# Kernel optimization log

Measured on AMD Instinct MI355X. Metric: run time of the kernel, lower is better.

The kernel has to match this reference:

```python
import jax, jax.numpy as jnp
import numpy as np

B, T, D, H, C = 2048, 512, 5, 128, 10  # batch, seq_len, input_dim, hidden_dim, num_classes


def setup_inputs() -> dict:
    key = jax.random.key(0)
    ks = jax.random.split(key, 13)
    s = 1.0 / np.sqrt(H)  # PyTorch LSTM init range

    def u(k, shape):
        return jax.random.uniform(k, shape, jnp.float32, -s, s)

    return {
        "x": jax.random.normal(ks[0], (B, T, D), jnp.float32),
        # layer 0 (gate order i,f,g,o as in PyTorch)
        "w_ih0": u(ks[1], (4 * H, D)),
        "w_hh0": u(ks[2], (4 * H, H)),
        "b_ih0": u(ks[3], (4 * H,)),
        "b_hh0": u(ks[4], (4 * H,)),
        # layer 1
        "w_ih1": u(ks[5], (4 * H, H)),
        "w_hh1": u(ks[6], (4 * H, H)),
        "b_ih1": u(ks[7], (4 * H,)),
        "b_hh1": u(ks[8], (4 * H,)),
        # classifier: Linear(H, H//2) -> ReLU -> Linear(H//2, C); dropout inactive (eval)
        "cw1": u(ks[9], (H // 2, H)),
        "cb1": u(ks[10], (H // 2,)),
        "cw2": u(ks[11], (C, H // 2)),
        "cb2": u(ks[12], (C,)),
    }


def _lstm_layer(xs, w_ih, w_hh, b_ih, b_hh):
    # xs: [T, B, in]; returns (ys [T, B, H], h_T [B, H])
    Hh = w_hh.shape[1]
    b = b_ih + b_hh

    def step(carry, x_t):
        h, c = carry
        gates = x_t @ w_ih.T + h @ w_hh.T + b  # [B, 4H]
        i, f, g, o = jnp.split(gates, 4, axis=-1)
        c = jax.nn.sigmoid(f) * c + jax.nn.sigmoid(i) * jnp.tanh(g)
        h = jax.nn.sigmoid(o) * jnp.tanh(c)
        return (h, c), h

    Bn = xs.shape[1]
    h0 = jnp.zeros((Bn, Hh), xs.dtype)
    (h_T, _), ys = jax.lax.scan(step, (h0, h0), xs)
    return ys, h_T


def reference(x, w_ih0, w_hh0, b_ih0, b_hh0, w_ih1, w_hh1, b_ih1, b_hh1, cw1, cb1, cw2, cb2):
    xs = jnp.transpose(x, (1, 0, 2))  # [T, B, D]
    ys0, _ = _lstm_layer(xs, w_ih0, w_hh0, b_ih0, b_hh0)
    # inter-layer dropout(0.2) is a no-op in eval mode
    _, last_hidden = _lstm_layer(ys0, w_ih1, w_hh1, b_ih1, b_hh1)  # h_n[-1]: [B, H]
    # classifier (Dropout(0.3) inactive in eval)
    r = jax.nn.relu(last_hidden @ cw1.T + cb1)
    output = r @ cw2.T + cb2  # [B, C]
    return (output, last_hidden)
```

## Files before the change

kernel.cpp:

```cpp
#include <hip/hip_runtime.h>

typedef unsigned short ushort;
typedef unsigned int uint;
typedef __bf16 bf16_t;
typedef bf16_t bf16x8 __attribute__((ext_vector_type(8)));
typedef float f32x4 __attribute__((ext_vector_type(4)));

#define B_ 2048
#define T_ 512
#define D_ 5
#define H_ 128
#define C_ 10
#define BT 16
#define BLK 512
#define NP 128
#define CH 8
#define H0STR 168
#define H1STR 136
#define SSTR 136
#define XSTR 40

static __device__ __forceinline__ float b2f(ushort u) {
    return __builtin_bit_cast(float, ((uint)u) << 16);
}
static __device__ __forceinline__ ushort f2b(float f) {
    uint u = __builtin_bit_cast(uint, f);
    u += 0x7FFFu + ((u >> 16) & 1u);
    return (ushort)(u >> 16);
}
static __device__ __forceinline__ float sigf(float x) {
    return __builtin_amdgcn_rcpf(1.0f + __expf(-x));
}
static __device__ __forceinline__ float tanhf_(float x) {
    return 1.0f - 2.0f * __builtin_amdgcn_rcpf(1.0f + __expf(2.0f * x));
}
static __device__ __forceinline__ float ldf(const void* p, long i, bool m32) {
    return m32 ? ((const float*)p)[i] : b2f(((const ushort*)p)[i]);
}
static __device__ __forceinline__ bf16x8 ld16(const ushort* p) {
    return __builtin_bit_cast(bf16x8, *(const uint4*)p);
}
static __device__ __forceinline__ bf16x8 ldfrag(const void* p, long idx, bool m32) {
    if (!m32) return ld16((const ushort*)p + idx);
    const float* f = (const float*)p + idx;
    union { ushort u[8]; bf16x8 v; } r;
#pragma unroll
    for (int j = 0; j < 8; ++j) r.u[j] = f2b(f[j]);
    return r.v;
}
static __device__ __forceinline__ f32x4 splat4(float v) {
    f32x4 r = {v, v, v, v};
    return r;
}
static __device__ __forceinline__ int swz(int row, int col) {
    return row * SSTR + ((((col >> 4) ^ (row >> 3)) << 4) | (col & 15));
}
static __device__ __forceinline__ void bar_lds() {
    asm volatile("s_waitcnt lgkmcnt(0)" ::: "memory");
    __builtin_amdgcn_s_barrier();
    asm volatile("" ::: "memory");
}

__global__ void detect_dtype(const ushort* __restrict__ w, int* __restrict__ flag) {
    __shared__ int cnt;
    if (threadIdx.x == 0) cnt = 0;
    __syncthreads();
    int local = 0;
    for (int i = threadIdx.x; i < 16384; i += 256)
        if ((uint)(w[i] & 0x7F80u) >= 0x4180u) ++local;
    atomicAdd(&cnt, local);
    __syncthreads();
    if (threadIdx.x == 0) *flag = (cnt > 512) ? 1 : 0;
}

__global__ void init_flags(int* __restrict__ prog) {
    prog[threadIdx.x] = 0;
}

__global__ __launch_bounds__(BLK, 2) void lstm2_pipe(
    const void* __restrict__ x,
    const void* __restrict__ wih0, const void* __restrict__ whh0,
    const void* __restrict__ bih0, const void* __restrict__ bhh0,
    const void* __restrict__ wih1, const void* __restrict__ whh1,
    const void* __restrict__ bih1, const void* __restrict__ bhh1,
    const void* __restrict__ cw1, const void* __restrict__ cb1,
    const void* __restrict__ cw2, const void* __restrict__ cb2,
    const int* __restrict__ flag,
    ushort* __restrict__ fifo, int* __restrict__ prog_p, int* __restrict__ prog_c,
    int F, void* __restrict__ out)
{
    __shared__ __align__(16) ushort sA[2][BT * SSTR];
    __shared__ __align__(16) ushort sB[2][BT * SSTR];
    __shared__ __align__(16) ushort xch[CH * 16 * XSTR];
    __shared__ float rs[BT * 64];

    const bool m32 = (*flag) != 0;
    const int tid  = threadIdx.x;
    const int w    = tid >> 6;
    const int lane = tid & 63;
    const int quad = lane >> 4;
    const int l16  = lane & 15;

    if ((int)blockIdx.x < NP) {
        const int p   = blockIdx.x;
        const int bt0 = p * BT;
        ushort* myfifo = fifo + (long)p * F * (BT * H_);

        const int e0 = tid;
        const int r0 = e0 / 40, rem0 = e0 - r0 * 40;
        const int tt0 = rem0 / 5, d0 = rem0 - tt0 * 5;
        const long xo0 = (long)(bt0 + r0) * T_ * D_ + (long)tt0 * D_ + d0;
        const int xdst0 = (tt0 * 16 + r0) * XSTR + d0;
        const int e1 = tid + 512;
        const int r1 = e1 / 40, rem1 = e1 - r1 * 40;
        const int tt1 = rem1 / 5, d1 = rem1 - tt1 * 5;
        const long xo1 = (long)(bt0 + r1) * T_ * D_ + (long)tt1 * D_ + d1;
        const int xdst1 = (tt1 * 16 + r1) * XSTR + d1;
        const bool has1 = (tid < 128);

        for (int i = tid; i < CH * 16 * XSTR; i += BLK) xch[i] = 0;

        bf16x8 wh0c[4][4];
        bf16x8 xbf[4];
        float  b0v[4];
#pragma unroll
        for (int g = 0; g < 4; ++g) {
            const int n = g * 128 + w * 16 + l16;
#pragma unroll
            for (int kt = 0; kt < 4; ++kt)
                wh0c[g][kt] = ldfrag(whh0, (long)n * 128 + kt * 32 + quad * 8, m32);
            union { ushort u[8]; bf16x8 v; } xt;
#pragma unroll
            for (int j = 0; j < 8; ++j) xt.u[j] = 0;
            if (quad == 0) {
#pragma unroll
                for (int j = 0; j < 5; ++j) xt.u[j] = f2b(ldf(wih0, (long)n * D_ + j, m32));
            }
            xbf[g] = xt.v;
            b0v[g] = ldf(bih0, n, m32) + ldf(bhh0, n, m32);
        }
        __syncthreads();

        {
            float v0 = ldf(x, xo0, m32);
            float v1 = has1 ? ldf(x, xo1, m32) : 0.f;
            xch[xdst0] = f2b(v0);
            if (has1) xch[xdst1] = f2b(v1);
        }
        float xp0 = ldf(x, xo0 + (long)(CH * D_), m32);
        float xp1 = has1 ? ldf(x, xo1 + (long)(CH * D_), m32) : 0.f;
        __syncthreads();

        bf16x8 h0f[4];
        {
            uint4 z = make_uint4(0, 0, 0, 0);
            h0f[0] = h0f[1] = h0f[2] = h0f[3] = __builtin_bit_cast(bf16x8, z);
        }
        f32x4 c0 = splat4(0.f);

#pragma unroll 1
        for (int t = 0; t < T_; ++t) {
            const int wb = (t + 1) & 1;
            if ((t & (CH - 1)) == 0 && t > 0) {
                __syncthreads();
                xch[xdst0] = f2b(xp0);
                if (has1) xch[xdst1] = f2b(xp1);
                if (tid == 0) {
                    __hip_atomic_store(&prog_p[p], t, __ATOMIC_RELEASE,
                                       __HIP_MEMORY_SCOPE_AGENT);
                    int need = t + CH - F;
                    if (need > 0)
                        while (__hip_atomic_load(&prog_c[p], __ATOMIC_RELAXED,
                                                 __HIP_MEMORY_SCOPE_AGENT) < need)
                            __builtin_amdgcn_s_sleep(2);
                }
                __syncthreads();
                const int tb = t + CH;
                xp0 = (tb + tt0 < T_) ? ldf(x, xo0 + (long)tb * D_, m32) : 0.f;
                xp1 = (has1 && tb + tt1 < T_) ? ldf(x, xo1 + (long)tb * D_, m32) : 0.f;
            }

            f32x4 a[4];
#pragma unroll
            for (int g = 0; g < 4; ++g) a[g] = splat4(b0v[g]);
#pragma unroll
            for (int kt = 0; kt < 4; ++kt)
#pragma unroll
                for (int g = 0; g < 4; ++g)
                    a[g] = __builtin_amdgcn_mfma_f32_16x16x32_bf16(
                        h0f[kt], wh0c[g][kt], a[g], 0, 0, 0);
            {
                bf16x8 ha4 = ld16(&xch[((t & (CH - 1)) * 16 + l16) * XSTR + quad * 8]);
#pragma unroll
                for (int g = 0; g < 4; ++g)
                    a[g] = __builtin_amdgcn_mfma_f32_16x16x32_bf16(
                        ha4, xbf[g], a[g], 0, 0, 0);
            }
            ushort* fs = myfifo + (long)(t & (F - 1)) * (BT * H_);
#pragma unroll
            for (int r = 0; r < 4; ++r) {
                float iv = sigf(a[0][r]), fv = sigf(a[1][r]);
                float gv = tanhf_(a[2][r]), ov = sigf(a[3][r]);
                float cv = fv * c0[r] + iv * gv;
                c0[r] = cv;
                ushort hv = f2b(ov * tanhf_(cv));
                int row = quad * 4 + r;
                sA[wb][swz(row, w * 16 + l16)] = hv;
                fs[row * H_ + w * 16 + l16] = hv;
            }
            bar_lds();
#pragma unroll
            for (int kt = 0; kt < 4; ++kt)
                h0f[kt] = ld16(&sA[wb][swz(l16, kt * 32 + quad * 8)]);
        }
        __syncthreads();
        if (tid == 0)
            __hip_atomic_store(&prog_p[p], T_, __ATOMIC_RELEASE,
                               __HIP_MEMORY_SCOPE_AGENT);
    } else {
        const int p   = blockIdx.x - NP;
        const int bt0 = p * BT;
        const ushort* myfifo = fifo + (long)p * F * (BT * H_);

        for (int i = tid; i < BT * SSTR; i += BLK) sB[0][i] = 0;

        bf16x8 wi1f[4][4], wh1f[4][4];
        float  b1v[4];
#pragma unroll
        for (int g = 0; g < 4; ++g) {
            const int n = g * 128 + w * 16 + l16;
#pragma unroll
            for (int kt = 0; kt < 4; ++kt) {
                wi1f[g][kt] = ldfrag(wih1, (long)n * 128 + kt * 32 + quad * 8, m32);
                wh1f[g][kt] = ldfrag(whh1, (long)n * 128 + kt * 32 + quad * 8, m32);
            }
            b1v[g] = ldf(bih1, n, m32) + ldf(bhh1, n, m32);
        }

        if (tid == 0) {
            while (__hip_atomic_load(&prog_p[p], __ATOMIC_RELAXED,
                                     __HIP_MEMORY_SCOPE_AGENT) < 2 * CH)
                __builtin_amdgcn_s_sleep(2);
            __builtin_amdgcn_fence(__ATOMIC_ACQUIRE, "agent");
        }
        __syncthreads();
        {
            int row = tid >> 5, col4 = (tid & 31) * 4;
            uint2 d = *(const uint2*)(myfifo + tid * 4);
            *(uint2*)&sA[0][swz(row, col4)] = d;
        }
        __syncthreads();

        f32x4 c1 = splat4(0.f);

#pragma unroll 1
        for (int t = 0; t < T_; ++t) {
            const int rb = t & 1, wb = (t + 1) & 1;
            if (((t + 1) & (CH - 1)) == 0 && t + 1 < T_) {
                if (tid == 0) {
                    int target = t + 1 + CH;
                    if (target > T_) target = T_;
                    while (__hip_atomic_load(&prog_p[p], __ATOMIC_RELAXED,
                                             __HIP_MEMORY_SCOPE_AGENT) < target)
                        __builtin_amdgcn_s_sleep(2);
                    __builtin_amdgcn_fence(__ATOMIC_ACQUIRE, "agent");
                    __hip_atomic_store(&prog_c[p], t + 1, __ATOMIC_RELEASE,
                                       __HIP_MEMORY_SCOPE_AGENT);
                }
                __syncthreads();
            }
            uint2 pf = make_uint2(0, 0);
            const bool hn = (t + 1 < T_);
            if (hn) pf = *(const uint2*)(myfifo
                          + (long)((t + 1) & (F - 1)) * (BT * H_) + tid * 4);

            f32x4 a[4];
#pragma unroll
            for (int g = 0; g < 4; ++g) a[g] = splat4(b1v[g]);
#pragma unroll
            for (int kt = 0; kt < 4; ++kt) {
                bf16x8 h0a = ld16(&sA[rb][swz(l16, kt * 32 + quad * 8)]);
#pragma unroll
                for (int g = 0; g < 4; ++g)
                    a[g] = __builtin_amdgcn_mfma_f32_16x16x32_bf16(
                        h0a, wi1f[g][kt], a[g], 0, 0, 0);
            }
#pragma unroll
            for (int kt = 0; kt < 4; ++kt) {
                bf16x8 hb = ld16(&sB[rb][swz(l16, kt * 32 + quad * 8)]);
#pragma unroll
                for (int g = 0; g < 4; ++g)
                    a[g] = __builtin_amdgcn_mfma_f32_16x16x32_bf16(
                        hb, wh1f[g][kt], a[g], 0, 0, 0);
            }
#pragma unroll
            for (int r = 0; r < 4; ++r) {
                float iv = sigf(a[0][r]), fv = sigf(a[1][r]);
                float gv = tanhf_(a[2][r]), ov = sigf(a[3][r]);
                float cv = fv * c1[r] + iv * gv;
                c1[r] = cv;
                sB[wb][swz(quad * 4 + r, w * 16 + l16)] = f2b(ov * tanhf_(cv));
            }
            if (hn) {
                int row = tid >> 5, col4 = (tid & 31) * 4;
                *(uint2*)&sA[wb][swz(row, col4)] = pf;
            }
            bar_lds();
        }

        if (tid < 256) {
            int m = tid >> 4, j0 = (tid & 15) * 4;
            float s0 = ldf(cb1, j0, m32), s1 = ldf(cb1, j0 + 1, m32);
            float s2 = ldf(cb1, j0 + 2, m32), s3 = ldf(cb1, j0 + 3, m32);
            const int mswz = m >> 3;
#pragma unroll
            for (int kb = 0; kb < 8; ++kb) {
                const ushort* hp = &sB[0][m * SSTR + ((kb ^ mswz) << 4)];
#pragma unroll
                for (int kk = 0; kk < 16; ++kk) {
                    int k = kb * 16 + kk;
                    float hv = b2f(hp[kk]);
                    s0 += hv * ldf(cw1, (long)j0 * 128 + k, m32);
                    s1 += hv * ldf(cw1, (long)(j0 + 1) * 128 + k, m32);
                    s2 += hv * ldf(cw1, (long)(j0 + 2) * 128 + k, m32);
                    s3 += hv * ldf(cw1, (long)(j0 + 3) * 128 + k, m32);
                }
            }
            rs[m * 64 + j0]     = fmaxf(s0, 0.f);
            rs[m * 64 + j0 + 1] = fmaxf(s1, 0.f);
            rs[m * 64 + j0 + 2] = fmaxf(s2, 0.f);
            rs[m * 64 + j0 + 3] = fmaxf(s3, 0.f);
        }
        __syncthreads();
        if (tid < 160) {
            int m = tid / 10, cc = tid - m * 10;
            float s = ldf(cb2, cc, m32);
#pragma unroll
            for (int j = 0; j < 64; ++j)
                s += rs[m * 64 + j] * ldf(cw2, (long)cc * 64 + j, m32);
            long oi = (long)(bt0 + m) * C_ + cc;
            if (m32) ((float*)out)[oi] = s; else ((ushort*)out)[oi] = f2b(s);
        }
        for (int idx = tid; idx < BT * H_; idx += BLK) {
            int m = idx >> 7, k = idx & 127;
            float v = b2f(sB[0][swz(m, k)]);
            long oi = (long)B_ * C_ + (long)(bt0 + m) * H_ + k;
            if (m32) ((float*)out)[oi] = v; else ((ushort*)out)[oi] = f2b(v);
        }
    }
}

__global__ __launch_bounds__(BLK, 2) void lstm2_mono(
    const void* __restrict__ x,
    const void* __restrict__ wih0, const void* __restrict__ whh0,
    const void* __restrict__ bih0, const void* __restrict__ bhh0,
    const void* __restrict__ wih1, const void* __restrict__ whh1,
    const void* __restrict__ bih1, const void* __restrict__ bhh1,
    const void* __restrict__ cw1, const void* __restrict__ cb1,
    const void* __restrict__ cw2, const void* __restrict__ cb2,
    const int* __restrict__ flag, void* __restrict__ out)
{
    __shared__ __align__(16) ushort h0s[2][BT * H0STR];
    __shared__ __align__(16) ushort h1s[2][BT * H1STR];
    __shared__ float rs[BT * 64];
    __shared__ uint4 xstash[4 * 8 * 64];

    const bool m32 = (*flag) != 0;
    const int tid  = threadIdx.x;
    const int w    = tid >> 6;
    const int lane = tid & 63;
    const int quad = lane >> 4;
    const int l16  = lane & 15;
    const int bt0  = blockIdx.x * BT;

    for (int i = tid; i < BT * 32; i += BLK) {
        int row = i >> 5, cc = i & 31;
        ushort v0 = (cc < 5) ? f2b(ldf(x, ((long)(bt0 + row) * T_) * D_ + cc, m32)) : (ushort)0;
        h0s[0][row * H0STR + 128 + cc] = v0;
        h0s[1][row * H0STR + 128 + cc] = 0;
    }
    for (int i = tid; i < BT * H_; i += BLK) {
        int row = i >> 7, cc = i & 127;
        h1s[1][row * H1STR + cc] = 0;
    }

    bf16x8 wh0c[4][4], wi1f[4][4], wh1f[4][4];
    float  b0v[4], b1v[4];
#pragma unroll
    for (int g = 0; g < 4; ++g) {
        const int n = g * 128 + w * 16 + l16;
#pragma unroll
        for (int kt = 0; kt < 4; ++kt) {
            wh0c[g][kt] = ldfrag(whh0, (long)n * 128 + kt * 32 + quad * 8, m32);
            wi1f[g][kt] = ldfrag(wih1, (long)n * 128 + kt * 32 + quad * 8, m32);
            wh1f[g][kt] = ldfrag(whh1, (long)n * 128 + kt * 32 + quad * 8, m32);
        }
        union { ushort u[8]; uint4 q; } xt;
        xt.q = make_uint4(0, 0, 0, 0);
        if (quad == 0) {
#pragma unroll
            for (int j = 0; j < 5; ++j) xt.u[j] = f2b(ldf(wih0, (long)n * D_ + j, m32));
        }
        xstash[(g * 8 + w) * 64 + lane] = xt.q;
        b0v[g] = ldf(bih0, n, m32) + ldf(bhh0, n, m32);
        b1v[g] = ldf(bih1, n, m32) + ldf(bhh1, n, m32);
    }
    __syncthreads();

    bf16x8 h0f[4];
    {
        uint4 z = make_uint4(0, 0, 0, 0);
        h0f[0] = h0f[1] = h0f[2] = h0f[3] = __builtin_bit_cast(bf16x8, z);
    }
    f32x4 c0 = splat4(0.f), c1 = splat4(0.f);
    const int xr = tid / 5, xc = tid - (tid / 5) * 5;

#pragma unroll 1
    for (int t = 0; t < T_; ++t) {
        const int wb = (t + 1) & 1, rb = t & 1;
        float xv = 0.f;
        const bool stage = (tid < 80) && (t < T_ - 1);
        if (stage) xv = ldf(x, ((long)(bt0 + xr) * T_ + (t + 1)) * D_ + xc, m32);

        f32x4 a[4];
#pragma unroll
        for (int g = 0; g < 4; ++g) a[g] = splat4(b0v[g]);
#pragma unroll
        for (int kt = 0; kt < 4; ++kt)
#pragma unroll
            for (int g = 0; g < 4; ++g)
                a[g] = __builtin_amdgcn_mfma_f32_16x16x32_bf16(
                    h0f[kt], wh0c[g][kt], a[g], 0, 0, 0);
        {
            bf16x8 ha4 = ld16(&h0s[rb][l16 * H0STR + 128 + quad * 8]);
#pragma unroll
            for (int g = 0; g < 4; ++g) {
                bf16x8 xb = __builtin_bit_cast(bf16x8, xstash[(g * 8 + w) * 64 + lane]);
                a[g] = __builtin_amdgcn_mfma_f32_16x16x32_bf16(ha4, xb, a[g], 0, 0, 0);
            }
        }
        ushort h0w[4];
#pragma unroll
        for (int r = 0; r < 4; ++r) {
            float iv = sigf(a[0][r]), fv = sigf(a[1][r]);
            float gv = tanhf_(a[2][r]), ov = sigf(a[3][r]);
            float cv = fv * c0[r] + iv * gv;
            c0[r] = cv;
            h0w[r] = f2b(ov * tanhf_(cv));
        }
#pragma unroll
        for (int r = 0; r < 4; ++r)
            h0s[wb][(quad * 4 + r) * H0STR + w * 16 + l16] = h0w[r];
        if (stage) h0s[wb][xr * H0STR + 128 + xc] = f2b(xv);
        __syncthreads();
#pragma unroll
        for (int kt = 0; kt < 4; ++kt)
            h0f[kt] = ld16(&h0s[wb][l16 * H0STR + kt * 32 + quad * 8]);

#pragma unroll
        for (int g = 0; g < 4; ++g) a[g] = splat4(b1v[g]);
#pragma unroll
        for (int kt = 0; kt < 4; ++kt)
#pragma unroll
            for (int g = 0; g < 4; ++g)
                a[g] = __builtin_amdgcn_mfma_f32_16x16x32_bf16(
                    h0f[kt], wi1f[g][kt], a[g], 0, 0, 0);
#pragma unroll
        for (int kt = 0; kt < 4; ++kt) {
            bf16x8 hb = ld16(&h1s[wb][l16 * H1STR + kt * 32 + quad * 8]);
#pragma unroll
            for (int g = 0; g < 4; ++g)
                a[g] = __builtin_amdgcn_mfma_f32_16x16x32_bf16(
                    hb, wh1f[g][kt], a[g], 0, 0, 0);
        }
#pragma unroll
        for (int r = 0; r < 4; ++r) {
            float iv = sigf(a[0][r]), fv = sigf(a[1][r]);
            float gv = tanhf_(a[2][r]), ov = sigf(a[3][r]);
            float cv = fv * c1[r] + iv * gv;
            c1[r] = cv;
            h1s[wb ^ 1][(quad * 4 + r) * H1STR + w * 16 + l16] = f2b(ov * tanhf_(cv));
        }
    }
    __syncthreads();

    if (tid < 256) {
        int m = tid >> 4, j0 = (tid & 15) * 4;
        float s0 = ldf(cb1, j0, m32), s1 = ldf(cb1, j0 + 1, m32);
        float s2 = ldf(cb1, j0 + 2, m32), s3 = ldf(cb1, j0 + 3, m32);
        const ushort* hr = &h1s[1][m * H1STR];
#pragma unroll 4
        for (int k = 0; k < 128; ++k) {
            float hv = b2f(hr[k]);
            s0 += hv * ldf(cw1, (long)j0 * 128 + k, m32);
            s1 += hv * ldf(cw1, (long)(j0 + 1) * 128 + k, m32);
            s2 += hv * ldf(cw1, (long)(j0 + 2) * 128 + k, m32);
            s3 += hv * ldf(cw1, (long)(j0 + 3) * 128 + k, m32);
        }
        rs[m * 64 + j0]     = fmaxf(s0, 0.f);
        rs[m * 64 + j0 + 1] = fmaxf(s1, 0.f);
        rs[m * 64 + j0 + 2] = fmaxf(s2, 0.f);
        rs[m * 64 + j0 + 3] = fmaxf(s3, 0.f);
    }
    __syncthreads();
    if (tid < 160) {
        int m = tid / 10, cc = tid - m * 10;
        float s = ldf(cb2, cc, m32);
#pragma unroll
        for (int j = 0; j < 64; ++j) s += rs[m * 64 + j] * ldf(cw2, (long)cc * 64 + j, m32);
        long oi = (long)(bt0 + m) * C_ + cc;
        if (m32) ((float*)out)[oi] = s; else ((ushort*)out)[oi] = f2b(s);
    }
    for (int idx = tid; idx < BT * H_; idx += BLK) {
        int m = idx >> 7, k = idx & 127;
        float v = b2f(h1s[1][m * H1STR + k]);
        long oi = (long)B_ * C_ + (long)(bt0 + m) * H_ + k;
        if (m32) ((float*)out)[oi] = v; else ((ushort*)out)[oi] = f2b(v);
    }
}

extern "C" void kernel_launch(void* const* d_in, const int* in_sizes, int n_in,
                              void* d_out, int out_size, void* d_ws, size_t ws_size,
                              hipStream_t stream) {
    (void)in_sizes; (void)n_in; (void)out_size;
    int* prog  = (int*)d_ws;
    int* flag  = (int*)((char*)d_ws + 4096);
    ushort* fifo = (ushort*)((char*)d_ws + 8192);

    hipLaunchKernelGGL(detect_dtype, dim3(1), dim3(256), 0, stream,
                       (const ushort*)d_in[2], flag);

    const size_t slot = (size_t)NP * BT * H_ * sizeof(ushort);
    int F = 0;
    if (ws_size >= 8192 + 64 * slot) F = 64;
    else if (ws_size >= 8192 + 32 * slot) F = 32;

    if (F) {
        hipLaunchKernelGGL(init_flags, dim3(1), dim3(256), 0, stream, prog);
        hipLaunchKernelGGL(lstm2_pipe, dim3(2 * NP), dim3(BLK), 0, stream,
                           d_in[0], d_in[1], d_in[2], d_in[3], d_in[4],
                           d_in[5], d_in[6], d_in[7], d_in[8],
                           d_in[9], d_in[10], d_in[11], d_in[12],
                           (const int*)flag, fifo, prog, prog + NP, F, d_out);
    } else {
        hipLaunchKernelGGL(lstm2_mono, dim3(B_ / BT), dim3(BLK), 0, stream,
                           d_in[0], d_in[1], d_in[2], d_in[3], d_in[4],
                           d_in[5], d_in[6], d_in[7], d_in[8],
                           d_in[9], d_in[10], d_in[11], d_in[12],
                           (const int*)flag, d_out);
    }
}
```

Baseline: 929.9 us.

## Precompute input-projection MFMAs off the recurrent critical path in both LSTM layers

In layer 0, the x-projection MFMA for step t+1 is now computed right after the h-fragment reload of step t, so the next step's recurrent MFMAs start from a bias-plus-input accumulator. In layer 1, the layer-0 hidden state for step t+1 is read straight from the global FIFO into MFMA fragments, bypassing the LDS staging buffer. Its W_ih projection is computed after the gate nonlinearities, ahead of the barrier. This shortens the dependency chain between consecutive timesteps. The cost is more live registers, which may add pressure or spills.

```diff
diff --git a/kernel.cpp b/kernel.cpp
--- a/kernel.cpp
+++ b/kernel.cpp
@@ -157,6 +157,17 @@
             h0f[0] = h0f[1] = h0f[2] = h0f[3] = __builtin_bit_cast(bf16x8, z);
         }
         f32x4 c0 = splat4(0.f);
+
+        f32x4 apre[4];
+        {
+            bf16x8 ha4 = ld16(&xch[(0 * 16 + l16) * XSTR + quad * 8]);
+#pragma unroll
+            for (int g = 0; g < 4; ++g) {
+                apre[g] = splat4(b0v[g]);
+                apre[g] = __builtin_amdgcn_mfma_f32_16x16x32_bf16(
+                    ha4, xbf[g], apre[g], 0, 0, 0);
+            }
+        }
 
 #pragma unroll 1
         for (int t = 0; t < T_; ++t) {
@@ -178,24 +189,25 @@
                 const int tb = t + CH;
                 xp0 = (tb + tt0 < T_) ? ldf(x, xo0 + (long)tb * D_, m32) : 0.f;
                 xp1 = (has1 && tb + tt1 < T_) ? ldf(x, xo1 + (long)tb * D_, m32) : 0.f;
+                bf16x8 ha4 = ld16(&xch[(0 * 16 + l16) * XSTR + quad * 8]);
+#pragma unroll
+                for (int g = 0; g < 4; ++g) {
+                    apre[g] = splat4(b0v[g]);
+                    apre[g] = __builtin_amdgcn_mfma_f32_16x16x32_bf16(
+                        ha4, xbf[g], apre[g], 0, 0, 0);
+                }
             }
 
             f32x4 a[4];
 #pragma unroll
-            for (int g = 0; g < 4; ++g) a[g] = splat4(b0v[g]);
+            for (int g = 0; g < 4; ++g) a[g] = apre[g];
 #pragma unroll
             for (int kt = 0; kt < 4; ++kt)
 #pragma unroll
                 for (int g = 0; g < 4; ++g)
                     a[g] = __builtin_amdgcn_mfma_f32_16x16x32_bf16(
                         h0f[kt], wh0c[g][kt], a[g], 0, 0, 0);
-            {
-                bf16x8 ha4 = ld16(&xch[((t & (CH - 1)) * 16 + l16) * XSTR + quad * 8]);
-#pragma unroll
-                for (int g = 0; g < 4; ++g)
-                    a[g] = __builtin_amdgcn_mfma_f32_16x16x32_bf16(
-                        ha4, xbf[g], a[g], 0, 0, 0);
-            }
+
             ushort* fs = myfifo + (long)(t & (F - 1)) * (BT * H_);
 #pragma unroll
             for (int r = 0; r < 4; ++r) {
@@ -212,6 +224,15 @@
 #pragma unroll
             for (int kt = 0; kt < 4; ++kt)
                 h0f[kt] = ld16(&sA[wb][swz(l16, kt * 32 + quad * 8)]);
+            if (t + 1 < T_ && ((t + 1) & (CH - 1)) != 0) {
+                bf16x8 ha4 = ld16(&xch[(((t + 1) & (CH - 1)) * 16 + l16) * XSTR + quad * 8]);
+#pragma unroll
+                for (int g = 0; g < 4; ++g) {
+                    apre[g] = splat4(b0v[g]);
+                    apre[g] = __builtin_amdgcn_mfma_f32_16x16x32_bf16(
+                        ha4, xbf[g], apre[g], 0, 0, 0);
+                }
+            }
         }
         __syncthreads();
         if (tid == 0)
@@ -244,14 +265,25 @@
             __builtin_amdgcn_fence(__ATOMIC_ACQUIRE, "agent");
         }
         __syncthreads();
-        {
-            int row = tid >> 5, col4 = (tid & 31) * 4;
-            uint2 d = *(const uint2*)(myfifo + tid * 4);
-            *(uint2*)&sA[0][swz(row, col4)] = d;
-        }
-        __syncthreads();
+
+        const long fragoff = (long)l16 * H_ + quad * 8;
+
+        bf16x8 h0a[4];
+#pragma unroll
+        for (int kt = 0; kt < 4; ++kt)
+            h0a[kt] = ld16(myfifo + fragoff + kt * 32);
 
         f32x4 c1 = splat4(0.f);
+
+        f32x4 apre[4];
+#pragma unroll
+        for (int g = 0; g < 4; ++g) apre[g] = splat4(b1v[g]);
+#pragma unroll
+        for (int kt = 0; kt < 4; ++kt)
+#pragma unroll
+            for (int g = 0; g < 4; ++g)
+                apre[g] = __builtin_amdgcn_mfma_f32_16x16x32_bf16(
+                    h0a[kt], wi1f[g][kt], apre[g], 0, 0, 0);
 
 #pragma unroll 1
         for (int t = 0; t < T_; ++t) {
@@ -269,22 +301,18 @@
                 }
                 __syncthreads();
             }
-            uint2 pf = make_uint2(0, 0);
             const bool hn = (t + 1 < T_);
-            if (hn) pf = *(const uint2*)(myfifo
-                          + (long)((t + 1) & (F - 1)) * (BT * H_) + tid * 4);
+            bf16x8 h0n[4];
+            if (hn) {
+                const ushort* fsrc = myfifo
+                    + (long)((t + 1) & (F - 1)) * (BT * H_) + fragoff;
+#pragma unroll
+                for (int kt = 0; kt < 4; ++kt) h0n[kt] = ld16(fsrc + kt * 32);
+            }
 
             f32x4 a[4];
 #pragma unroll
-            for (int g = 0; g < 4; ++g) a[g] = splat4(b1v[g]);
-#pragma unroll
-            for (int kt = 0; kt < 4; ++kt) {
-                bf16x8 h0a = ld16(&sA[rb][swz(l16, kt * 32 + quad * 8)]);
-#pragma unroll
-                for (int g = 0; g < 4; ++g)
-                    a[g] = __builtin_amdgcn_mfma_f32_16x16x32_bf16(
-                        h0a, wi1f[g][kt], a[g], 0, 0, 0);
-            }
+            for (int g = 0; g < 4; ++g) a[g] = apre[g];
 #pragma unroll
             for (int kt = 0; kt < 4; ++kt) {
                 bf16x8 hb = ld16(&sB[rb][swz(l16, kt * 32 + quad * 8)]);
@@ -302,8 +330,16 @@
                 sB[wb][swz(quad * 4 + r, w * 16 + l16)] = f2b(ov * tanhf_(cv));
             }
             if (hn) {
-                int row = tid >> 5, col4 = (tid & 31) * 4;
-                *(uint2*)&sA[wb][swz(row, col4)] = pf;
+#pragma unroll
+                for (int kt = 0; kt < 4; ++kt) h0a[kt] = h0n[kt];
+#pragma unroll
+                for (int g = 0; g < 4; ++g) apre[g] = splat4(b1v[g]);
+#pragma unroll
+                for (int kt = 0; kt < 4; ++kt)
+#pragma unroll
+                    for (int g = 0; g < 4; ++g)
+                        apre[g] = __builtin_amdgcn_mfma_f32_16x16x32_bf16(
+                            h0a[kt], wi1f[g][kt], apre[g], 0, 0, 0);
             }
             bar_lds();
         }
```

After: 1.059 ms. 1.14x slower.

## Fuse both LSTM layers into one block with wave-specialized skewed pipeline

Applied to the files above, without the earlier changes.

Replaces the two-kernel-group producer/consumer design, which passed layer-0 outputs through a global FIFO guarded by atomic flags, with a single fused kernel. Inside each block, waves 0-3 compute layer 0 and waves 4-7 compute layer 1 one timestep behind, handing data over through double-buffered LDS with a single barrier per step. Layer-1 input weights are staged in swizzled dynamic shared memory, while recurrent weights stay in registers. This removes global-memory handoff and spin-wait overhead, but each block now runs both layers with half the waves per layer and relies on a large LDS allocation, which may limit occupancy.

```diff
diff --git a/kernel.cpp b/kernel.cpp
--- a/kernel.cpp
+++ b/kernel.cpp
@@ -13,12 +13,17 @@
 #define C_ 10
 #define BT 16
 #define BLK 512
-#define NP 128
 #define CH 8
-#define H0STR 168
-#define H1STR 136
-#define SSTR 136
+#define HSTR 136
 #define XSTR 40
+
+#define WI1OFF 0
+#define SA0 65536
+#define SA1 (SA0 + 2176)
+#define SB0 (SA0 + 4352)
+#define SB1 (SA0 + 6528)
+#define XCHO (SA0 + 8704)
+#define LDS_USH (XCHO + 5120)
 
 static __device__ __forceinline__ float b2f(ushort u) {
     return __builtin_bit_cast(float, ((uint)u) << 16);
@@ -52,9 +57,6 @@
     f32x4 r = {v, v, v, v};
     return r;
 }
-static __device__ __forceinline__ int swz(int row, int col) {
-    return row * SSTR + ((((col >> 4) ^ (row >> 3)) << 4) | (col & 15));
-}
 static __device__ __forceinline__ void bar_lds() {
     asm volatile("s_waitcnt lgkmcnt(0)" ::: "memory");
     __builtin_amdgcn_s_barrier();
@@ -73,284 +75,7 @@
     if (threadIdx.x == 0) *flag = (cnt > 512) ? 1 : 0;
 }
 
-__global__ void init_flags(int* __restrict__ prog) {
-    prog[threadIdx.x] = 0;
-}
-
-__global__ __launch_bounds__(BLK, 2) void lstm2_pipe(
-    const void* __restrict__ x,
-    const void* __restrict__ wih0, const void* __restrict__ whh0,
-    const void* __restrict__ bih0, const void* __restrict__ bhh0,
-    const void* __restrict__ wih1, const void* __restrict__ whh1,
-    const void* __restrict__ bih1, const void* __restrict__ bhh1,
-    const void* __restrict__ cw1, const void* __restrict__ cb1,
-    const void* __restrict__ cw2, const void* __restrict__ cb2,
-    const int* __restrict__ flag,
-    ushort* __restrict__ fifo, int* __restrict__ prog_p, int* __restrict__ prog_c,
-    int F, void* __restrict__ out)
-{
-    __shared__ __align__(16) ushort sA[2][BT * SSTR];
-    __shared__ __align__(16) ushort sB[2][BT * SSTR];
-    __shared__ __align__(16) ushort xch[CH * 16 * XSTR];
-    __shared__ float rs[BT * 64];
-
-    const bool m32 = (*flag) != 0;
-    const int tid  = threadIdx.x;
-    const int w    = tid >> 6;
-    const int lane = tid & 63;
-    const int quad = lane >> 4;
-    const int l16  = lane & 15;
-
-    if ((int)blockIdx.x < NP) {
-        const int p   = blockIdx.x;
-        const int bt0 = p * BT;
-        ushort* myfifo = fifo + (long)p * F * (BT * H_);
-
-        const int e0 = tid;
-        const int r0 = e0 / 40, rem0 = e0 - r0 * 40;
-        const int tt0 = rem0 / 5, d0 = rem0 - tt0 * 5;
-        const long xo0 = (long)(bt0 + r0) * T_ * D_ + (long)tt0 * D_ + d0;
-        const int xdst0 = (tt0 * 16 + r0) * XSTR + d0;
-        const int e1 = tid + 512;
-        const int r1 = e1 / 40, rem1 = e1 - r1 * 40;
-        const int tt1 = rem1 / 5, d1 = rem1 - tt1 * 5;
-        const long xo1 = (long)(bt0 + r1) * T_ * D_ + (long)tt1 * D_ + d1;
-        const int xdst1 = (tt1 * 16 + r1) * XSTR + d1;
-        const bool has1 = (tid < 128);
-
-        for (int i = tid; i < CH * 16 * XSTR; i += BLK) xch[i] = 0;
-
-        bf16x8 wh0c[4][4];
-        bf16x8 xbf[4];
-        float  b0v[4];
-#pragma unroll
-        for (int g = 0; g < 4; ++g) {
-            const int n = g * 128 + w * 16 + l16;
-#pragma unroll
-            for (int kt = 0; kt < 4; ++kt)
-                wh0c[g][kt] = ldfrag(whh0, (long)n * 128 + kt * 32 + quad * 8, m32);
-            union { ushort u[8]; bf16x8 v; } xt;
-#pragma unroll
-            for (int j = 0; j < 8; ++j) xt.u[j] = 0;
-            if (quad == 0) {
-#pragma unroll
-                for (int j = 0; j < 5; ++j) xt.u[j] = f2b(ldf(wih0, (long)n * D_ + j, m32));
-            }
-            xbf[g] = xt.v;
-            b0v[g] = ldf(bih0, n, m32) + ldf(bhh0, n, m32);
-        }
-        __syncthreads();
-
-        {
-            float v0 = ldf(x, xo0, m32);
-            float v1 = has1 ? ldf(x, xo1, m32) : 0.f;
-            xch[xdst0] = f2b(v0);
-            if (has1) xch[xdst1] = f2b(v1);
-        }
-        float xp0 = ldf(x, xo0 + (long)(CH * D_), m32);
-        float xp1 = has1 ? ldf(x, xo1 + (long)(CH * D_), m32) : 0.f;
-        __syncthreads();
-
-        bf16x8 h0f[4];
-        {
-            uint4 z = make_uint4(0, 0, 0, 0);
-            h0f[0] = h0f[1] = h0f[2] = h0f[3] = __builtin_bit_cast(bf16x8, z);
-        }
-        f32x4 c0 = splat4(0.f);
-
-#pragma unroll 1
-        for (int t = 0; t < T_; ++t) {
-            const int wb = (t + 1) & 1;
-            if ((t & (CH - 1)) == 0 && t > 0) {
-                __syncthreads();
-                xch[xdst0] = f2b(xp0);
-                if (has1) xch[xdst1] = f2b(xp1);
-                if (tid == 0) {
-                    __hip_atomic_store(&prog_p[p], t, __ATOMIC_RELEASE,
-                                       __HIP_MEMORY_SCOPE_AGENT);
-                    int need = t + CH - F;
-                    if (need > 0)
-                        while (__hip_atomic_load(&prog_c[p], __ATOMIC_RELAXED,
-                                                 __HIP_MEMORY_SCOPE_AGENT) < need)
-                            __builtin_amdgcn_s_sleep(2);
-                }
-                __syncthreads();
-                const int tb = t + CH;
-                xp0 = (tb + tt0 < T_) ? ldf(x, xo0 + (long)tb * D_, m32) : 0.f;
-                xp1 = (has1 && tb + tt1 < T_) ? ldf(x, xo1 + (long)tb * D_, m32) : 0.f;
-            }
-
-            f32x4 a[4];
-#pragma unroll
-            for (int g = 0; g < 4; ++g) a[g] = splat4(b0v[g]);
-#pragma unroll
-            for (int kt = 0; kt < 4; ++kt)
-#pragma unroll
-                for (int g = 0; g < 4; ++g)
-                    a[g] = __builtin_amdgcn_mfma_f32_16x16x32_bf16(
-                        h0f[kt], wh0c[g][kt], a[g], 0, 0, 0);
-            {
-                bf16x8 ha4 = ld16(&xch[((t & (CH - 1)) * 16 + l16) * XSTR + quad * 8]);
-#pragma unroll
-                for (int g = 0; g < 4; ++g)
-                    a[g] = __builtin_amdgcn_mfma_f32_16x16x32_bf16(
-                        ha4, xbf[g], a[g], 0, 0, 0);
-            }
-            ushort* fs = myfifo + (long)(t & (F - 1)) * (BT * H_);
-#pragma unroll
-            for (int r = 0; r < 4; ++r) {
-                float iv = sigf(a[0][r]), fv = sigf(a[1][r]);
-                float gv = tanhf_(a[2][r]), ov = sigf(a[3][r]);
-                float cv = fv * c0[r] + iv * gv;
-                c0[r] = cv;
-                ushort hv = f2b(ov * tanhf_(cv));
-                int row = quad * 4 + r;
-                sA[wb][swz(row, w * 16 + l16)] = hv;
-                fs[row * H_ + w * 16 + l16] = hv;
-            }
-            bar_lds();
-#pragma unroll
-            for (int kt = 0; kt < 4; ++kt)
-                h0f[kt] = ld16(&sA[wb][swz(l16, kt * 32 + quad * 8)]);
-        }
-        __syncthreads();
-        if (tid == 0)
-            __hip_atomic_store(&prog_p[p], T_, __ATOMIC_RELEASE,
-                               __HIP_MEMORY_SCOPE_AGENT);
-    } else {
-        const int p   = blockIdx.x - NP;
-        const int bt0 = p * BT;
-        const ushort* myfifo = fifo + (long)p * F * (BT * H_);
-
-        for (int i = tid; i < BT * SSTR; i += BLK) sB[0][i] = 0;
-
-        bf16x8 wi1f[4][4], wh1f[4][4];
-        float  b1v[4];
-#pragma unroll
-        for (int g = 0; g < 4; ++g) {
-            const int n = g * 128 + w * 16 + l16;
-#pragma unroll
-            for (int kt = 0; kt < 4; ++kt) {
-                wi1f[g][kt] = ldfrag(wih1, (long)n * 128 + kt * 32 + quad * 8, m32);
-                wh1f[g][kt] = ldfrag(whh1, (long)n * 128 + kt * 32 + quad * 8, m32);
-            }
-            b1v[g] = ldf(bih1, n, m32) + ldf(bhh1, n, m32);
-        }
-
-        if (tid == 0) {
-            while (__hip_atomic_load(&prog_p[p], __ATOMIC_RELAXED,
-                                     __HIP_MEMORY_SCOPE_AGENT) < 2 * CH)
-                __builtin_amdgcn_s_sleep(2);
-            __builtin_amdgcn_fence(__ATOMIC_ACQUIRE, "agent");
-        }
-        __syncthreads();
-        {
-            int row = tid >> 5, col4 = (tid & 31) * 4;
-            uint2 d = *(const uint2*)(myfifo + tid * 4);
-            *(uint2*)&sA[0][swz(row, col4)] = d;
-        }
-        __syncthreads();
-
-        f32x4 c1 = splat4(0.f);
-
-#pragma unroll 1
-        for (int t = 0; t < T_; ++t) {
-            const int rb = t & 1, wb = (t + 1) & 1;
-            if (((t + 1) & (CH - 1)) == 0 && t + 1 < T_) {
-                if (tid == 0) {
-                    int target = t + 1 + CH;
-                    if (target > T_) target = T_;
-                    while (__hip_atomic_load(&prog_p[p], __ATOMIC_RELAXED,
-                                             __HIP_MEMORY_SCOPE_AGENT) < target)
-                        __builtin_amdgcn_s_sleep(2);
-                    __builtin_amdgcn_fence(__ATOMIC_ACQUIRE, "agent");
-                    __hip_atomic_store(&prog_c[p], t + 1, __ATOMIC_RELEASE,
-                                       __HIP_MEMORY_SCOPE_AGENT);
-                }
-                __syncthreads();
-            }
-            uint2 pf = make_uint2(0, 0);
-            const bool hn = (t + 1 < T_);
-            if (hn) pf = *(const uint2*)(myfifo
-                          + (long)((t + 1) & (F - 1)) * (BT * H_) + tid * 4);
-
-            f32x4 a[4];
-#pragma unroll
-            for (int g = 0; g < 4; ++g) a[g] = splat4(b1v[g]);
-#pragma unroll
-            for (int kt = 0; kt < 4; ++kt) {
-                bf16x8 h0a = ld16(&sA[rb][swz(l16, kt * 32 + quad * 8)]);
-#pragma unroll
-                for (int g = 0; g < 4; ++g)
-                    a[g] = __builtin_amdgcn_mfma_f32_16x16x32_bf16(
-                        h0a, wi1f[g][kt], a[g], 0, 0, 0);
-            }
-#pragma unroll
-            for (int kt = 0; kt < 4; ++kt) {
-                bf16x8 hb = ld16(&sB[rb][swz(l16, kt * 32 + quad * 8)]);
-#pragma unroll
-                for (int g = 0; g < 4; ++g)
-                    a[g] = __builtin_amdgcn_mfma_f32_16x16x32_bf16(
-                        hb, wh1f[g][kt], a[g], 0, 0, 0);
-            }
-#pragma unroll
-            for (int r = 0; r < 4; ++r) {
-                float iv = sigf(a[0][r]), fv = sigf(a[1][r]);
-                float gv = tanhf_(a[2][r]), ov = sigf(a[3][r]);
-                float cv = fv * c1[r] + iv * gv;
-                c1[r] = cv;
-                sB[wb][swz(quad * 4 + r, w * 16 + l16)] = f2b(ov * tanhf_(cv));
-            }
-            if (hn) {
-                int row = tid >> 5, col4 = (tid & 31) * 4;
-                *(uint2*)&sA[wb][swz(row, col4)] = pf;
-            }
-            bar_lds();
-        }
-
-        if (tid < 256) {
-            int m = tid >> 4, j0 = (tid & 15) * 4;
-            float s0 = ldf(cb1, j0, m32), s1 = ldf(cb1, j0 + 1, m32);
-            float s2 = ldf(cb1, j0 + 2, m32), s3 = ldf(cb1, j0 + 3, m32);
-            const int mswz = m >> 3;
-#pragma unroll
-            for (int kb = 0; kb < 8; ++kb) {
-                const ushort* hp = &sB[0][m * SSTR + ((kb ^ mswz) << 4)];
-#pragma unroll
-                for (int kk = 0; kk < 16; ++kk) {
-                    int k = kb * 16 + kk;
-                    float hv = b2f(hp[kk]);
-                    s0 += hv * ldf(cw1, (long)j0 * 128 + k, m32);
-                    s1 += hv * ldf(cw1, (long)(j0 + 1) * 128 + k, m32);
-                    s2 += hv * ldf(cw1, (long)(j0 + 2) * 128 + k, m32);
-                    s3 += hv * ldf(cw1, (long)(j0 + 3) * 128 + k, m32);
-                }
-            }
-            rs[m * 64 + j0]     = fmaxf(s0, 0.f);
-            rs[m * 64 + j0 + 1] = fmaxf(s1, 0.f);
-            rs[m * 64 + j0 + 2] = fmaxf(s2, 0.f);
-            rs[m * 64 + j0 + 3] = fmaxf(s3, 0.f);
-        }
-        __syncthreads();
-        if (tid < 160) {
-            int m = tid / 10, cc = tid - m * 10;
-            float s = ldf(cb2, cc, m32);
-#pragma unroll
-            for (int j = 0; j < 64; ++j)
-                s += rs[m * 64 + j] * ldf(cw2, (long)cc * 64 + j, m32);
-            long oi = (long)(bt0 + m) * C_ + cc;
-            if (m32) ((float*)out)[oi] = s; else ((ushort*)out)[oi] = f2b(s);
-        }
-        for (int idx = tid; idx < BT * H_; idx += BLK) {
-            int m = idx >> 7, k = idx & 127;
-            float v = b2f(sB[0][swz(m, k)]);
-            long oi = (long)B_ * C_ + (long)(bt0 + m) * H_ + k;
-            if (m32) ((float*)out)[oi] = v; else ((ushort*)out)[oi] = f2b(v);
-        }
-    }
-}
-
-__global__ __launch_bounds__(BLK, 2) void lstm2_mono(
+__global__ __launch_bounds__(BLK, 2) void lstm2_fused(
     const void* __restrict__ x,
     const void* __restrict__ wih0, const void* __restrict__ whh0,
     const void* __restrict__ bih0, const void* __restrict__ bhh0,
@@ -360,10 +85,7 @@
     const void* __restrict__ cw2, const void* __restrict__ cb2,
     const int* __restrict__ flag, void* __restrict__ out)
 {
-    __shared__ __align__(16) ushort h0s[2][BT * H0STR];
-    __shared__ __align__(16) ushort h1s[2][BT * H1STR];
-    __shared__ float rs[BT * 64];
-    __shared__ uint4 xstash[4 * 8 * 64];
+    extern __shared__ __align__(16) ushort lds[];
 
     const bool m32 = (*flag) != 0;
     const int tid  = threadIdx.x;
@@ -372,123 +94,183 @@
     const int quad = lane >> 4;
     const int l16  = lane & 15;
     const int bt0  = blockIdx.x * BT;
-
-    for (int i = tid; i < BT * 32; i += BLK) {
-        int row = i >> 5, cc = i & 31;
-        ushort v0 = (cc < 5) ? f2b(ldf(x, ((long)(bt0 + row) * T_) * D_ + cc, m32)) : (ushort)0;
-        h0s[0][row * H0STR + 128 + cc] = v0;
-        h0s[1][row * H0STR + 128 + cc] = 0;
-    }
-    for (int i = tid; i < BT * H_; i += BLK) {
-        int row = i >> 7, cc = i & 127;
-        h1s[1][row * H1STR + cc] = 0;
-    }
-
-    bf16x8 wh0c[4][4], wi1f[4][4], wh1f[4][4];
-    float  b0v[4], b1v[4];
-#pragma unroll
-    for (int g = 0; g < 4; ++g) {
-        const int n = g * 128 + w * 16 + l16;
-#pragma unroll
-        for (int kt = 0; kt < 4; ++kt) {
-            wh0c[g][kt] = ldfrag(whh0, (long)n * 128 + kt * 32 + quad * 8, m32);
-            wi1f[g][kt] = ldfrag(wih1, (long)n * 128 + kt * 32 + quad * 8, m32);
-            wh1f[g][kt] = ldfrag(whh1, (long)n * 128 + kt * 32 + quad * 8, m32);
-        }
-        union { ushort u[8]; uint4 q; } xt;
-        xt.q = make_uint4(0, 0, 0, 0);
-        if (quad == 0) {
-#pragma unroll
-            for (int j = 0; j < 5; ++j) xt.u[j] = f2b(ldf(wih0, (long)n * D_ + j, m32));
-        }
-        xstash[(g * 8 + w) * 64 + lane] = xt.q;
-        b0v[g] = ldf(bih0, n, m32) + ldf(bhh0, n, m32);
-        b1v[g] = ldf(bih1, n, m32) + ldf(bhh1, n, m32);
-    }
-    __syncthreads();
-
-    bf16x8 h0f[4];
-    {
-        uint4 z = make_uint4(0, 0, 0, 0);
-        h0f[0] = h0f[1] = h0f[2] = h0f[3] = __builtin_bit_cast(bf16x8, z);
-    }
-    f32x4 c0 = splat4(0.f), c1 = splat4(0.f);
-    const int xr = tid / 5, xc = tid - (tid / 5) * 5;
-
-#pragma unroll 1
-    for (int t = 0; t < T_; ++t) {
-        const int wb = (t + 1) & 1, rb = t & 1;
-        float xv = 0.f;
-        const bool stage = (tid < 80) && (t < T_ - 1);
-        if (stage) xv = ldf(x, ((long)(bt0 + xr) * T_ + (t + 1)) * D_ + xc, m32);
-
-        f32x4 a[4];
-#pragma unroll
-        for (int g = 0; g < 4; ++g) a[g] = splat4(b0v[g]);
-#pragma unroll
-        for (int kt = 0; kt < 4; ++kt)
-#pragma unroll
-            for (int g = 0; g < 4; ++g)
-                a[g] = __builtin_amdgcn_mfma_f32_16x16x32_bf16(
-                    h0f[kt], wh0c[g][kt], a[g], 0, 0, 0);
-        {
-            bf16x8 ha4 = ld16(&h0s[rb][l16 * H0STR + 128 + quad * 8]);
-#pragma unroll
-            for (int g = 0; g < 4; ++g) {
-                bf16x8 xb = __builtin_bit_cast(bf16x8, xstash[(g * 8 + w) * 64 + lane]);
-                a[g] = __builtin_amdgcn_mfma_f32_16x16x32_bf16(ha4, xb, a[g], 0, 0, 0);
+    const bool isL0 = (w < 4);
+    const int  cb   = (w & 3) * 32;
+
+    for (int i2 = tid; i2 < 2176; i2 += BLK) { lds[SA1 + i2] = 0; lds[SB1 + i2] = 0; }
+    for (int i2 = tid; i2 < 5120; i2 += BLK) lds[XCHO + i2] = 0;
+
+    for (int f = tid; f < 8192; f += BLK) {
+        int n = f >> 4, k0 = (f & 15) << 3;
+        bf16x8 v = ldfrag(wih1, (long)n * 128 + k0, m32);
+        int us = (k0 >> 5) * 16384 + n * 32 + ((k0 & 31) ^ ((n & 3) << 3));
+        *(uint4*)&lds[us] = __builtin_bit_cast(uint4, v);
+    }
+
+    const int e0 = tid;
+    const int r0 = e0 / 40, rem0 = e0 - r0 * 40;
+    const int tt0 = rem0 / 5, d0 = rem0 - tt0 * 5;
+    const long xo0 = (long)(bt0 + r0) * T_ * D_ + (long)tt0 * D_ + d0;
+    const int xdst0 = (tt0 * 16 + r0) * XSTR + d0;
+    const int e1 = tid + 512;
+    const int r1 = e1 / 40, rem1 = e1 - r1 * 40;
+    const int tt1 = rem1 / 5, d1 = rem1 - tt1 * 5;
+    const long xo1 = (long)(bt0 + r1) * T_ * D_ + (long)tt1 * D_ + d1;
+    const int xdst1 = (tt1 * 16 + r1) * XSTR + d1;
+    const bool has1 = (tid < 128);
+
+    bf16x8 wreg[2][4][4];
+    bf16x8 xbf[2][4];
+    float  bv[2][4];
+    int    ibase[2][4];
+#pragma unroll
+    for (int nt = 0; nt < 2; ++nt)
+#pragma unroll
+        for (int g = 0; g < 4; ++g) {
+            const int n = g * 128 + cb + nt * 16 + l16;
+            if (isL0) {
+#pragma unroll
+                for (int kt = 0; kt < 4; ++kt)
+                    wreg[nt][g][kt] = ldfrag(whh0, (long)n * 128 + kt * 32 + quad * 8, m32);
+                union { ushort u[8]; bf16x8 v; } xt;
+#pragma unroll
+                for (int j = 0; j < 8; ++j) xt.u[j] = 0;
+                if (quad == 0) {
+#pragma unroll
+                    for (int j = 0; j < 5; ++j)
+                        xt.u[j] = f2b(ldf(wih0, (long)n * D_ + j, m32));
+                }
+                xbf[nt][g] = xt.v;
+                bv[nt][g] = ldf(bih0, n, m32) + ldf(bhh0, n, m32);
+                ibase[nt][g] = 0;
+            } else {
+#pragma unroll
+                for (int kt = 0; kt < 4; ++kt)
+                    wreg[nt][g][kt] = ldfrag(whh1, (long)n * 128 + kt * 32 + quad * 8, m32);
+                bv[nt][g] = ldf(bih1, n, m32) + ldf(bhh1, n, m32);
+                ibase[nt][g] = n * 32 + ((quad * 8) ^ ((l16 & 3) << 3));
             }
         }
-        ushort h0w[4];
-#pragma unroll
-        for (int r = 0; r < 4; ++r) {
-            float iv = sigf(a[0][r]), fv = sigf(a[1][r]);
-            float gv = tanhf_(a[2][r]), ov = sigf(a[3][r]);
-            float cv = fv * c0[r] + iv * gv;
-            c0[r] = cv;
-            h0w[r] = f2b(ov * tanhf_(cv));
+    __syncthreads();
+
+    {
+        float v0 = ldf(x, xo0, m32);
+        lds[XCHO + xdst0] = f2b(v0);
+        if (has1) { float v1 = ldf(x, xo1, m32); lds[XCHO + xdst1] = f2b(v1); }
+    }
+    float xp0 = ldf(x, xo0 + (long)(CH * D_), m32);
+    float xp1 = has1 ? ldf(x, xo1 + (long)(CH * D_), m32) : 0.f;
+    __syncthreads();
+
+    f32x4 cst[2];
+    cst[0] = splat4(0.f);
+    cst[1] = splat4(0.f);
+
+#pragma unroll 1
+    for (int i = 0; i <= T_; ++i) {
+        const int pb = i & 1;
+        if (i > 0 && i < T_ && (i & (CH - 1)) == 0) {
+            lds[XCHO + xdst0] = f2b(xp0);
+            if (has1) lds[XCHO + xdst1] = f2b(xp1);
+            bar_lds();
+            const int tb = i + CH;
+            xp0 = (tb + tt0 < T_) ? ldf(x, xo0 + (long)tb * D_, m32) : 0.f;
+            xp1 = (has1 && tb + tt1 < T_) ? ldf(x, xo1 + (long)tb * D_, m32) : 0.f;
         }
-#pragma unroll
-        for (int r = 0; r < 4; ++r)
-            h0s[wb][(quad * 4 + r) * H0STR + w * 16 + l16] = h0w[r];
-        if (stage) h0s[wb][xr * H0STR + 128 + xc] = f2b(xv);
-        __syncthreads();
-#pragma unroll
-        for (int kt = 0; kt < 4; ++kt)
-            h0f[kt] = ld16(&h0s[wb][l16 * H0STR + kt * 32 + quad * 8]);
-
-#pragma unroll
-        for (int g = 0; g < 4; ++g) a[g] = splat4(b1v[g]);
-#pragma unroll
-        for (int kt = 0; kt < 4; ++kt)
-#pragma unroll
-            for (int g = 0; g < 4; ++g)
-                a[g] = __builtin_amdgcn_mfma_f32_16x16x32_bf16(
-                    h0f[kt], wi1f[g][kt], a[g], 0, 0, 0);
-#pragma unroll
-        for (int kt = 0; kt < 4; ++kt) {
-            bf16x8 hb = ld16(&h1s[wb][l16 * H1STR + kt * 32 + quad * 8]);
-#pragma unroll
-            for (int g = 0; g < 4; ++g)
-                a[g] = __builtin_amdgcn_mfma_f32_16x16x32_bf16(
-                    hb, wh1f[g][kt], a[g], 0, 0, 0);
+        const int rdA = pb ? SA0 : SA1;
+        if (isL0) {
+            if (i < T_) {
+                bf16x8 hf[4];
+#pragma unroll
+                for (int kt = 0; kt < 4; ++kt)
+                    hf[kt] = ld16(&lds[rdA + l16 * HSTR + kt * 32 + quad * 8]);
+                bf16x8 xa = ld16(&lds[XCHO + ((i & 7) * 16 + l16) * XSTR + quad * 8]);
+                f32x4 a[2][4];
+#pragma unroll
+                for (int nt = 0; nt < 2; ++nt)
+#pragma unroll
+                    for (int g = 0; g < 4; ++g) {
+                        a[nt][g] = splat4(bv[nt][g]);
+                        a[nt][g] = __builtin_amdgcn_mfma_f32_16x16x32_bf16(
+                            xa, xbf[nt][g], a[nt][g], 0, 0, 0);
+                    }
+#pragma unroll
+                for (int kt = 0; kt < 4; ++kt)
+#pragma unroll
+                    for (int nt = 0; nt < 2; ++nt)
+#pragma unroll
+                        for (int g = 0; g < 4; ++g)
+                            a[nt][g] = __builtin_amdgcn_mfma_f32_16x16x32_bf16(
+                                hf[kt], wreg[nt][g][kt], a[nt][g], 0, 0, 0);
+                const int wrA = pb ? SA1 : SA0;
+#pragma unroll
+                for (int nt = 0; nt < 2; ++nt)
+#pragma unroll
+                    for (int r = 0; r < 4; ++r) {
+                        float iv = sigf(a[nt][0][r]), fv = sigf(a[nt][1][r]);
+                        float gv = tanhf_(a[nt][2][r]), ov = sigf(a[nt][3][r]);
+                        float cv = fv * cst[nt][r] + iv * gv;
+                        cst[nt][r] = cv;
+                        lds[wrA + (quad * 4 + r) * HSTR + cb + nt * 16 + l16] =
+                            f2b(ov * tanhf_(cv));
+                    }
+            }
+        } else {
+            if (i >= 1) {
+                const int rdB = pb ? SB1 : SB0;
+                const int wrB = pb ? SB0 : SB1;
+                bf16x8 h0a[4], hb[4];
+#pragma unroll
+                for (int kt = 0; kt < 4; ++kt)
+                    h0a[kt] = ld16(&lds[rdA + l16 * HSTR + kt * 32 + quad * 8]);
+#pragma unroll
+                for (int kt = 0; kt < 4; ++kt)
+                    hb[kt] = ld16(&lds[rdB + l16 * HSTR + kt * 32 + quad * 8]);
+                f32x4 a[2][4];
+#pragma unroll
+                for (int nt = 0; nt < 2; ++nt)
+#pragma unroll
+                    for (int g = 0; g < 4; ++g) a[nt][g] = splat4(bv[nt][g]);
+#pragma unroll
+                for (int kt = 0; kt < 4; ++kt)
+#pragma unroll
+                    for (int nt = 0; nt < 2; ++nt)
+#pragma unroll
+                        for (int g = 0; g < 4; ++g) {
+                            bf16x8 wf = ld16(&lds[kt * 16384 + ibase[nt][g]]);
+                            a[nt][g] = __builtin_amdgcn_mfma_f32_16x16x32_bf16(
+                                h0a[kt], wf, a[nt][g], 0, 0, 0);
+                        }
+#pragma unroll
+                for (int kt = 0; kt < 4; ++kt)
+#pragma unroll
+                    for (int nt = 0; nt < 2; ++nt)
+#pragma unroll
+                        for (int g = 0; g < 4; ++g)
+                            a[nt][g] = __builtin_amdgcn_mfma_f32_16x16x32_bf16(
+                                hb[kt], wreg[nt][g][kt], a[nt][g], 0, 0, 0);
+#pragma unroll
+                for (int nt = 0; nt < 2; ++nt)
+#pragma unroll
+                    for (int r = 0; r < 4; ++r) {
+                        float iv = sigf(a[nt][0][r]), fv = sigf(a[nt][1][r]);
+                        float gv = tanhf_(a[nt][2][r]), ov = sigf(a[nt][3][r]);
+                        float cv = fv * cst[nt][r] + iv * gv;
+                        cst[nt][r] = cv;
+                        lds[wrB + (quad * 4 + r) * HSTR + cb + nt * 16 + l16] =
+                            f2b(ov * tanhf_(cv));
+                    }
+            }
         }
-#pragma unroll
-        for (int r = 0; r < 4; ++r) {
-            float iv = sigf(a[0][r]), fv = sigf(a[1][r]);
-            float gv = tanhf_(a[2][r]), ov = sigf(a[3][r]);
-            float cv = fv * c1[r] + iv * gv;
-            c1[r] = cv;
-            h1s[wb ^ 1][(quad * 4 + r) * H1STR + w * 16 + l16] = f2b(ov * tanhf_(cv));
-        }
-    }
-    __syncthreads();
-
+        bar_lds();
+    }
+
+    float* rs = (float*)&lds[XCHO];
     if (tid < 256) {
         int m = tid >> 4, j0 = (tid & 15) * 4;
         float s0 = ldf(cb1, j0, m32), s1 = ldf(cb1, j0 + 1, m32);
         float s2 = ldf(cb1, j0 + 2, m32), s3 = ldf(cb1, j0 + 3, m32);
-        const ushort* hr = &h1s[1][m * H1STR];
+        const ushort* hr = &lds[SB1 + m * HSTR];
 #pragma unroll 4
         for (int k = 0; k < 128; ++k) {
             float hv = b2f(hr[k]);
@@ -507,13 +289,14 @@
         int m = tid / 10, cc = tid - m * 10;
         float s = ldf(cb2, cc, m32);
 #pragma unroll
-        for (int j = 0; j < 64; ++j) s += rs[m * 64 + j] * ldf(cw2, (long)cc * 64 + j, m32);
+        for (int j = 0; j < 64; ++j)
+            s += rs[m * 64 + j] * ldf(cw2, (long)cc * 64 + j, m32);
         long oi = (long)(bt0 + m) * C_ + cc;
         if (m32) ((float*)out)[oi] = s; else ((ushort*)out)[oi] = f2b(s);
     }
     for (int idx = tid; idx < BT * H_; idx += BLK) {
         int m = idx >> 7, k = idx & 127;
-        float v = b2f(h1s[1][m * H1STR + k]);
+        float v = b2f(lds[SB1 + m * HSTR + k]);
         long oi = (long)B_ * C_ + (long)(bt0 + m) * H_ + k;
         if (m32) ((float*)out)[oi] = v; else ((ushort*)out)[oi] = f2b(v);
     }
@@ -522,31 +305,23 @@
 extern "C" void kernel_launch(void* const* d_in, const int* in_sizes, int n_in,
                               void* d_out, int out_size, void* d_ws, size_t ws_size,
                               hipStream_t stream) {
-    (void)in_sizes; (void)n_in; (void)out_size;
-    int* prog  = (int*)d_ws;
-    int* flag  = (int*)((char*)d_ws + 4096);
-    ushort* fifo = (ushort*)((char*)d_ws + 8192);
+    (void)in_sizes; (void)n_in; (void)out_size; (void)ws_size;
+    int* flag = (int*)d_ws;
+
+    static int attr_done = 0;
+    if (!attr_done) {
+        (void)hipFuncSetAttribute((const void*)lstm2_fused,
+                                  hipFuncAttributeMaxDynamicSharedMemorySize,
+                                  LDS_USH * 2);
+        attr_done = 1;
+    }
 
     hipLaunchKernelGGL(detect_dtype, dim3(1), dim3(256), 0, stream,
                        (const ushort*)d_in[2], flag);
 
-    const size_t slot = (size_t)NP * BT * H_ * sizeof(ushort);
-    int F = 0;
-    if (ws_size >= 8192 + 64 * slot) F = 64;
-    else if (ws_size >= 8192 + 32 * slot) F = 32;
-
-    if (F) {
-        hipLaunchKernelGGL(init_flags, dim3(1), dim3(256), 0, stream, prog);
-        hipLaunchKernelGGL(lstm2_pipe, dim3(2 * NP), dim3(BLK), 0, stream,
-                           d_in[0], d_in[1], d_in[2], d_in[3], d_in[4],
-                           d_in[5], d_in[6], d_in[7], d_in[8],
-                           d_in[9], d_in[10], d_in[11], d_in[12],
-                           (const int*)flag, fifo, prog, prog + NP, F, d_out);
-    } else {
-        hipLaunchKernelGGL(lstm2_mono, dim3(B_ / BT), dim3(BLK), 0, stream,
-                           d_in[0], d_in[1], d_in[2], d_in[3], d_in[4],
-                           d_in[5], d_in[6], d_in[7], d_in[8],
-                           d_in[9], d_in[10], d_in[11], d_in[12],
-                           (const int*)flag, d_out);
-    }
-}
+    hipLaunchKernelGGL(lstm2_fused, dim3(B_ / BT), dim3(BLK), LDS_USH * 2, stream,
+                       d_in[0], d_in[1], d_in[2], d_in[3], d_in[4],
+                       d_in[5], d_in[6], d_in[7], d_in[8],
+                       d_in[9], d_in[10], d_in[11], d_in[12],
+                       (const int*)flag, d_out);
+}
```

Result: slower. 1.861 ms (+100.1%).
